# Kernel tuning notes

Hardware: AMD Instinct MI355X
Metric: run time of the kernel (lower is better)

The kernel has to match this reference:

```python
import jax, jax.numpy as jnp
import numpy as np

B, L, D = 2, 2048, 2048
H, KVH, Dh = 16, 8, 128
S_ROPE = 1024
EPS = 1e-5


def rms_norm(x, w):
    xf = x.astype(jnp.float32)
    xf = xf * jax.lax.rsqrt(jnp.mean(xf * xf, axis=-1, keepdims=True) + EPS)
    return (xf * w).astype(x.dtype)


def rotate_half(x):
    x1, x2 = jnp.split(x, 2, axis=-1)
    return jnp.concatenate((-x2, x1), axis=-1)


def setup_inputs() -> dict:
    key = jax.random.key(0)
    ks = jax.random.split(key, 12)
    sc = 0.02
    # 1D rope tables at every absolute position (theta = 500000 as in config)
    inv_freq = 1.0 / (500000.0 ** (np.arange(0, Dh, 2, dtype=np.float32) / Dh))
    ang = np.arange(L, dtype=np.float32)[:, None] * inv_freq[None, :]  # [L, Dh/2]
    emb = np.concatenate([ang, ang], axis=-1)  # [L, Dh]
    # 3D rope as per-pair 2x2 rotation matrices
    ang3 = np.random.RandomState(0).uniform(-np.pi, np.pi, size=(S_ROPE, Dh // 2)).astype(np.float32)
    R = np.stack([np.stack([np.cos(ang3), -np.sin(ang3)], -1),
                  np.stack([np.sin(ang3), np.cos(ang3)], -1)], -2)  # [S,Dh/2,2,2]
    mpos = jnp.array([[[128, 1025], [1160, 513]],
                      [[128, 1025], [1160, 513]]], dtype=jnp.int64)
    return {
        "hidden_states": jax.random.normal(ks[0], (B, L, D), jnp.float32),
        "temb": jax.random.normal(ks[1], (B, D), jnp.float32),
        "w_ln": jnp.ones((D,), jnp.float32),
        "w_mod": jax.random.normal(ks[2], (D, 3 * D), jnp.float32) * sc,
        "b_mod": jnp.zeros((3 * D,), jnp.float32),
        "wq": jax.random.normal(ks[3], (D, H * Dh), jnp.float32) * sc,
        "wk": jax.random.normal(ks[4], (D, KVH * Dh), jnp.float32) * sc,
        "wv": jax.random.normal(ks[5], (D, KVH * Dh), jnp.float32) * sc,
        "wo": jax.random.normal(ks[6], (H * Dh, D), jnp.float32) * sc,
        "qn_w": jnp.ones((Dh,), jnp.float32),
        "kn_w": jnp.ones((Dh,), jnp.float32),
        "cos_1d": jnp.asarray(np.cos(emb)),
        "sin_1d": jnp.asarray(np.sin(emb)),
        "rope_3d": jnp.asarray(R),
        "modality_positions": mpos,
    }


def _masks(modality_positions):
    pos = jnp.arange(L)  # [L]
    off = modality_positions[..., 0]   # [B, S]
    ln = modality_positions[..., 1]    # [B, S]
    meta = 1  # add_time_embeds=True, add_ar_embeds=False
    seg_end = off + jnp.maximum(ln, meta)
    in_full = (pos[None, None, :] >= off[..., None]) & (pos[None, None, :] < seg_end[..., None])
    text_mask = ~jnp.any(in_full, axis=1)  # [B, L]
    img_start = off + meta
    in_img = (pos[None, None, :] >= img_start[..., None]) & (pos[None, None, :] < (off + ln)[..., None])
    rel = jnp.sum(jnp.where(in_img, pos[None, None, :] - img_start[..., None], 0), axis=1)  # [B, L]
    img_mask = jnp.any(in_img, axis=1) & (rel < S_ROPE) & (rel >= 0)
    rel = jnp.clip(rel, 0, S_ROPE - 1)
    return text_mask, img_mask, rel


def _apply_mixed_rope(q, k, cos_1d, sin_1d, rope_3d, text_mask, img_mask, rel):
    # text 1D rope (rotate_half style), applied at absolute position
    c = cos_1d[None, None]  # [1,1,L,Dh]
    s = sin_1d[None, None]
    q_txt = q * c + rotate_half(q) * s
    k_txt = k * c + rotate_half(k) * s
    # image 3D rope: per-pair 2x2 rotation gathered at within-image index
    R = rope_3d[rel]  # [B, L, Dh/2, 2, 2]
    q2 = q.reshape(*q.shape[:-1], Dh // 2, 2)
    k2 = k.reshape(*k.shape[:-1], Dh // 2, 2)
    q_img = jnp.einsum('bhlpi,blpij->bhlpj', q2, R).reshape(q.shape)
    k_img = jnp.einsum('bhlpi,blpij->bhlpj', k2, R).reshape(k.shape)
    mt = text_mask[:, None, :, None]
    mi = img_mask[:, None, :, None]
    q_out = jnp.where(mt, q_txt, jnp.where(mi, q_img, q))
    k_out = jnp.where(mt, k_txt, jnp.where(mi, k_img, k))
    return q_out, k_out


def reference(hidden_states, temb, w_ln, w_mod, b_mod, wq, wk, wv, wo,
              qn_w, kn_w, cos_1d, sin_1d, rope_3d, modality_positions):
    dtype = hidden_states.dtype
    # adaLN modulation
    mod = jax.nn.silu(temb) @ w_mod + b_mod  # [B, 3D]
    shift, scale, gate = jnp.split(mod, 3, axis=-1)
    xn = rms_norm(hidden_states, w_ln)
    xm = (xn.astype(jnp.float32) * (1.0 + scale[:, None, :].astype(jnp.float32))
          + shift[:, None, :].astype(jnp.float32)).astype(dtype)
    # qkv projections (GQA)
    q = (xm @ wq).reshape(B, L, H, Dh).transpose(0, 2, 1, 3)
    k = (xm @ wk).reshape(B, L, KVH, Dh).transpose(0, 2, 1, 3)
    v = (xm @ wv).reshape(B, L, KVH, Dh).transpose(0, 2, 1, 3)
    # qk-norm over head_dim
    q = rms_norm(q, qn_w)
    k = rms_norm(k, kn_w)
    # mixed 3D-image / 1D-text RoPE
    text_mask, img_mask, rel = _masks(modality_positions)
    q, k = _apply_mixed_rope(q, k, cos_1d, sin_1d, rope_3d, text_mask, img_mask, rel)
    # GQA: repeat kv heads (repeat_interleave along head dim)
    n_rep = H // KVH
    k = jnp.repeat(k, n_rep, axis=1)
    v = jnp.repeat(v, n_rep, axis=1)
    # full attention (no causal mask for diffusion block)
    scores = jnp.einsum('bhqd,bhkd->bhqk', q, k) / jnp.sqrt(jnp.asarray(Dh, q.dtype))
    attn = jax.nn.softmax(scores, axis=-1)
    o = jnp.einsum('bhqk,bhkd->bhqd', attn, v)
    o = o.transpose(0, 2, 1, 3).reshape(B, L, H * Dh) @ wo
    return hidden_states + gate[:, None, :].astype(dtype) * o


if __name__ == '__main__':
    out = reference(**setup_inputs())
    print(out.shape, out.dtype)
```

## Files before the change

### kernel.cpp

```cpp
#include <hip/hip_runtime.h>
#include <stdint.h>
#include <math.h>

typedef unsigned short u16;
typedef __attribute__((ext_vector_type(8))) short short8;
typedef __attribute__((ext_vector_type(4))) float fx4;
typedef __attribute__((ext_vector_type(4))) unsigned short u16x4;

#define DEV __device__ __forceinline__

DEV u16 f2bf(float f) {
  unsigned u = __builtin_bit_cast(unsigned, f);
  return (u16)((u + 0x7FFFu + ((u >> 16) & 1u)) >> 16);
}
DEV float bf2f(u16 h) { return __builtin_bit_cast(float, ((unsigned)h) << 16); }

DEV fx4 mfma16(short8 a, short8 b, fx4 c) {
  return __builtin_amdgcn_mfma_f32_16x16x32_bf16(a, b, c, 0, 0, 0);
}

#if __has_builtin(__builtin_amdgcn_exp2f)
DEV float exp2v(float x) { return __builtin_amdgcn_exp2f(x); }
#else
DEV float exp2v(float x) { return exp2f(x); }
#endif

#define GLD16(g, l)                                                            \
  __builtin_amdgcn_global_load_lds(                                            \
      (const __attribute__((address_space(1))) void*)(g),                      \
      (__attribute__((address_space(3))) void*)(l), 16, 0, 0)

#define WAIT_ALL() asm volatile("s_waitcnt vmcnt(0) lgkmcnt(0)" ::: "memory")

__global__ __launch_bounds__(512) void k_silu_mod(
    const float* __restrict__ temb, const float* __restrict__ wmod,
    const float* __restrict__ bmod, float* __restrict__ mod) {
  __shared__ float st[4096];
  __shared__ float red[8][2][64];
  int tid = threadIdx.x;
  for (int i = tid; i < 4096; i += 512) {
    float t = temb[i];
    st[i] = t / (1.0f + __expf(-t));
  }
  __syncthreads();
  int j = blockIdx.x * 64 + (tid & 63);
  int ks = tid >> 6;
  float a0 = 0.f, a1 = 0.f;
  for (int d = ks * 256; d < ks * 256 + 256; ++d) {
    float w = wmod[(size_t)d * 6144 + j];
    a0 += st[d] * w;
    a1 += st[2048 + d] * w;
  }
  red[ks][0][tid & 63] = a0;
  red[ks][1][tid & 63] = a1;
  __syncthreads();
  if (tid < 64) {
    float s0 = 0.f, s1 = 0.f;
#pragma unroll
    for (int i = 0; i < 8; ++i) {
      s0 += red[i][0][tid];
      s1 += red[i][1][tid];
    }
    mod[j] = s0 + bmod[j];
    mod[6144 + j] = s1 + bmod[j];
  }
}

__global__ __launch_bounds__(256) void k_xm(
    const float* __restrict__ x, const float* __restrict__ wln,
    const float* __restrict__ mod, u16* __restrict__ xm) {
  int row = blockIdx.x;
  int b = row >> 11;
  const float* xr = x + (size_t)row * 2048;
  int tid = threadIdx.x;
  float4 v0 = ((const float4*)xr)[tid];
  float4 v1 = ((const float4*)xr)[tid + 256];
  float ss = v0.x * v0.x + v0.y * v0.y + v0.z * v0.z + v0.w * v0.w +
             v1.x * v1.x + v1.y * v1.y + v1.z * v1.z + v1.w * v1.w;
  for (int m = 1; m < 64; m <<= 1) ss += __shfl_xor(ss, m);
  __shared__ float red[4];
  if ((tid & 63) == 0) red[tid >> 6] = ss;
  __syncthreads();
  ss = red[0] + red[1] + red[2] + red[3];
  float r = rsqrtf(ss * (1.0f / 2048.0f) + 1e-5f);
  const float* mb = mod + (size_t)b * 6144;
#pragma unroll
  for (int c = 0; c < 2; ++c) {
    int j0 = (tid + c * 256) * 4;
    float4 xv = c ? v1 : v0;
    float4 sh = *(const float4*)(mb + j0);
    float4 sc = *(const float4*)(mb + 2048 + j0);
    float4 wl = *(const float4*)(wln + j0);
    u16x4 o;
    o.x = f2bf(xv.x * r * wl.x * (1.f + sc.x) + sh.x);
    o.y = f2bf(xv.y * r * wl.y * (1.f + sc.y) + sh.y);
    o.z = f2bf(xv.z * r * wl.z * (1.f + sc.z) + sh.z);
    o.w = f2bf(xv.w * r * wl.w * (1.f + sc.w) + sh.w);
    *(u16x4*)(xm + (size_t)row * 2048 + j0) = o;
  }
}

__global__ __launch_bounds__(256) void k_tconv(
    const float* __restrict__ src, u16* __restrict__ dst, int cols, int rows) {
  __shared__ float t[32][33];
  int kb = blockIdx.x * 32, nb = blockIdx.y * 32;
  int tx = threadIdx.x, ty = threadIdx.y;
#pragma unroll
  for (int i = 0; i < 4; ++i)
    t[ty + i * 8][tx] = src[(size_t)(kb + ty + i * 8) * cols + nb + tx];
  __syncthreads();
#pragma unroll
  for (int i = 0; i < 4; ++i)
    dst[(size_t)(nb + ty + i * 8) * rows + kb + tx] = f2bf(t[tx][ty + i * 8]);
}

template <int EPI>
__global__ __launch_bounds__(256) void k_gemm(
    const u16* __restrict__ A, const u16* __restrict__ Bt, void* __restrict__ Cp,
    const float* __restrict__ hid, const float* __restrict__ mod, int N, int K) {
  __shared__ u16 As[128 * 32];
  __shared__ u16 Bs[128 * 32];
  int tid = threadIdx.x;
  int wave = tid >> 6, lane = tid & 63, quad = lane >> 4, l16 = lane & 15;
  int m0 = blockIdx.y * 128, n0 = blockIdx.x * 128;
  int wm = (wave >> 1) * 64, wn = (wave & 1) * 64;
  fx4 acc[4][4] = {};
  int rowa = tid >> 2;
  int chunk = (tid & 3) ^ ((rowa >> 1) & 3);
  int cola = chunk * 8;
  const u16* Ag = A + (size_t)(m0 + rowa) * K + cola;
  const u16* Bg = Bt + (size_t)(n0 + rowa) * K + cola;
  u16* AsW = &As[wave * 512];
  u16* BsW = &Bs[wave * 512];
  int sl = (quad ^ ((l16 >> 1) & 3)) * 8;
  for (int k0 = 0; k0 < K; k0 += 32) {
    GLD16(Ag + k0, AsW);
    GLD16(Ag + k0 + (size_t)64 * K, AsW + 2048);
    GLD16(Bg + k0, BsW);
    GLD16(Bg + k0 + (size_t)64 * K, BsW + 2048);
    __syncthreads();
    short8 af[4], bfr[4];
#pragma unroll
    for (int i = 0; i < 4; ++i) {
      af[i] = *(const short8*)&As[(wm + i * 16 + l16) * 32 + sl];
      bfr[i] = *(const short8*)&Bs[(wn + i * 16 + l16) * 32 + sl];
    }
#pragma unroll
    for (int i = 0; i < 4; ++i)
#pragma unroll
      for (int j = 0; j < 4; ++j) acc[i][j] = mfma16(af[i], bfr[j], acc[i][j]);
    __syncthreads();
  }
#pragma unroll
  for (int i = 0; i < 4; ++i) {
    int row = m0 + wm + i * 16 + quad * 4;
#pragma unroll
    for (int j = 0; j < 4; ++j) {
      int col = n0 + wn + j * 16 + l16;
      if (EPI == 0) {
        u16* C = (u16*)Cp;
#pragma unroll
        for (int r = 0; r < 4; ++r)
          C[(size_t)(row + r) * N + col] = f2bf(acc[i][j][r]);
      } else {
        float* C = (float*)Cp;
        int b = row >> 11;
        float g = mod[(size_t)b * 6144 + 4096 + col];
#pragma unroll
        for (int r = 0; r < 4; ++r)
          C[(size_t)(row + r) * N + col] =
              hid[(size_t)(row + r) * N + col] + g * acc[i][j][r];
      }
    }
  }
}

__global__ __launch_bounds__(192) void k_qknorm(
    const u16* __restrict__ qkv, const float* __restrict__ qn,
    const float* __restrict__ kn, const float* __restrict__ cos1,
    const float* __restrict__ sin1, const float* __restrict__ r3,
    const int* __restrict__ mpos, u16* __restrict__ Q, u16* __restrict__ Kb) {
  int bx = blockIdx.x;
  int b = bx >> 11, l = bx & 2047;
  int tid = threadIdx.x;
  int slot = tid >> 3, sub = tid & 7;
  bool isq = slot < 16;
  int head = isq ? slot : slot - 16;
  const u16* base = qkv + (size_t)bx * 4096 + (isq ? slot * 128 : 2048 + head * 128);
  int d0 = sub * 16;
  float xv[16];
#pragma unroll
  for (int i = 0; i < 16; ++i) xv[i] = bf2f(base[d0 + i]);
  float ss = 0.f;
#pragma unroll
  for (int i = 0; i < 16; ++i) ss += xv[i] * xv[i];
  ss += __shfl_xor(ss, 1);
  ss += __shfl_xor(ss, 2);
  ss += __shfl_xor(ss, 4);
  float r = rsqrtf(ss * (1.0f / 128.0f) + 1e-5f);
  int mp[8];
  {
    bool is64 = (mpos[1] == 0) & (mpos[3] == 0) & (mpos[5] == 0) & (mpos[7] == 0);
#pragma unroll
    for (int i = 0; i < 8; ++i) mp[i] = is64 ? mpos[2 * i] : mpos[i];
  }
  bool infull = false, inimg = false;
  int rel = 0;
#pragma unroll
  for (int s = 0; s < 2; ++s) {
    int off = mp[b * 4 + s * 2], ln = mp[b * 4 + s * 2 + 1];
    int mx = ln > 1 ? ln : 1;
    infull |= (l >= off) && (l < off + mx);
    bool ii = (l >= off + 1) && (l < off + ln);
    inimg |= ii;
    rel += ii ? (l - (off + 1)) : 0;
  }
  bool text = !infull;
  bool img = inimg && (rel < 1024);
  const float* w = isq ? qn : kn;
  float out[16];
  if (text) {
    int dp0 = d0 ^ 64;
    float sgn = (d0 < 64) ? -1.f : 1.f;
#pragma unroll
    for (int i = 0; i < 16; ++i) {
      int d = d0 + i, dp = dp0 + i;
      float c = cos1[(size_t)l * 128 + d];
      float s = sin1[(size_t)l * 128 + d];
      float xp = bf2f(base[dp]);
      out[i] = r * (xv[i] * w[d] * c + sgn * xp * w[dp] * s);
    }
  } else if (img) {
    const float* R = r3 + ((size_t)rel * 64 + (d0 >> 1)) * 4;
#pragma unroll
    for (int p = 0; p < 8; ++p) {
      float a = xv[2 * p] * w[d0 + 2 * p] * r;
      float c2 = xv[2 * p + 1] * w[d0 + 2 * p + 1] * r;
      out[2 * p] = a * R[4 * p + 0] + c2 * R[4 * p + 2];
      out[2 * p + 1] = a * R[4 * p + 1] + c2 * R[4 * p + 3];
    }
  } else {
#pragma unroll
    for (int i = 0; i < 16; ++i) out[i] = xv[i] * w[d0 + i] * r;
  }
  if (isq) {
    u16* dst = Q + ((size_t)(b * 16 + head) * 2048 + l) * 128 + d0;
#pragma unroll
    for (int i = 0; i < 16; ++i)
      dst[i] = f2bf(out[i] * (0.08838834764831845f * 1.4426950408889634f));
  } else {
    u16* dst = Kb + ((size_t)(b * 8 + head) * 2048 + l) * 128 + d0;
#pragma unroll
    for (int i = 0; i < 16; ++i) dst[i] = f2bf(out[i]);
  }
}

__global__ __launch_bounds__(256) void k_vtrans(const u16* __restrict__ qkv,
                                                u16* __restrict__ VT) {
  __shared__ u16 t[64][65];
  int bh = blockIdx.x;
  int l0 = blockIdx.y * 64, d0 = blockIdx.z * 64;
  int b = bh >> 3, kvh = bh & 7;
  int tx = threadIdx.x & 63, tg = threadIdx.x >> 6;
#pragma unroll
  for (int i = 0; i < 16; ++i) {
    int li = tg + i * 4;
    t[li][tx] = qkv[(size_t)(b * 2048 + l0 + li) * 4096 + 3072 + kvh * 128 + d0 + tx];
  }
  __syncthreads();
#pragma unroll
  for (int i = 0; i < 16; ++i) {
    int di = tg + i * 4;
    VT[((size_t)bh * 128 + d0 + di) * 2048 + l0 + tx] = t[tx][di];
  }
}

__global__ __launch_bounds__(512, 4) void k_attn(
    const u16* __restrict__ Q, const u16* __restrict__ Kb,
    const u16* __restrict__ VT, u16* __restrict__ O) {
  __shared__ u16 Ks[2][64 * 128];
  __shared__ u16 Vs[2][128 * 64];
  __shared__ u16 Ps[128 * 64];
  int tid = threadIdx.x;
  int wave = tid >> 6, lane = tid & 63, quad = lane >> 4, l16 = lane & 15;
  int bh = blockIdx.y;
  int b = bh >> 4, h = bh & 15, kvh = h >> 1;
  int q0 = blockIdx.x * 128;
  const u16* Qb = Q + ((size_t)bh * 2048 + q0 + wave * 16) * 128;
  short8 qf[4];
#pragma unroll
  for (int ks = 0; ks < 4; ++ks)
    qf[ks] = *(const short8*)(Qb + l16 * 128 + ks * 32 + quad * 8);
  const u16* Kg = Kb + (size_t)(b * 8 + kvh) * 2048 * 128;
  const u16* Vg = VT + (size_t)(b * 8 + kvh) * 128 * 2048;
  float mrow[4], lpart[4];
  fx4 of[8] = {};
#pragma unroll
  for (int r = 0; r < 4; ++r) {
    mrow[r] = -INFINITY;
    lpart[r] = 0.f;
  }
  size_t kgo[2], vgo[2];
#pragma unroll
  for (int i = 0; i < 2; ++i) {
    int kr = i * 32 + wave * 4 + (lane >> 4);
    kgo[i] = (size_t)kr * 128 + (((lane & 15) ^ (kr & 15)) * 8);
    int vr = i * 64 + wave * 8 + (lane >> 3);
    vgo[i] = (size_t)vr * 2048 + (((lane & 7) ^ (vr & 7)) * 8);
  }

  auto STAGE = [&](int t, int buf) {
    size_t ko = (size_t)t * 8192;
    size_t vo = (size_t)t * 64;
#pragma unroll
    for (int i = 0; i < 2; ++i) {
      GLD16(Kg + ko + kgo[i], &Ks[buf][i * 4096 + wave * 512]);
      GLD16(Vg + vo + vgo[i], &Vs[buf][i * 4096 + wave * 512]);
    }
  };

  auto COMPUTE = [&](int buf) {
    fx4 sf[4] = {};
    __builtin_amdgcn_s_setprio(1);
#pragma unroll
    for (int ct = 0; ct < 4; ++ct) {
#pragma unroll
      for (int ks = 0; ks < 4; ++ks) {
        short8 kf = *(const short8*)&Ks[buf][(ct * 16 + l16) * 128 +
                                            (((ks * 4 + quad) ^ l16) * 8)];
        sf[ct] = mfma16(qf[ks], kf, sf[ct]);
      }
    }
    __builtin_amdgcn_s_setprio(0);
    float cmv[4];
    bool need = false;
#pragma unroll
    for (int r = 0; r < 4; ++r) {
      cmv[r] = fmaxf(fmaxf(sf[0][r], sf[1][r]), fmaxf(sf[2][r], sf[3][r]));
      need |= (cmv[r] > mrow[r] + 8.0f);
    }
    if (__any(need)) {
#pragma unroll
      for (int r = 0; r < 4; ++r) {
        float cm = cmv[r];
        cm = fmaxf(cm, __shfl_xor(cm, 1));
        cm = fmaxf(cm, __shfl_xor(cm, 2));
        cm = fmaxf(cm, __shfl_xor(cm, 4));
        cm = fmaxf(cm, __shfl_xor(cm, 8));
        float mn = fmaxf(mrow[r], cm);
        float al = exp2v(mrow[r] - mn);
        mrow[r] = mn;
        lpart[r] *= al;
#pragma unroll
        for (int c2 = 0; c2 < 8; ++c2) of[c2][r] *= al;
      }
    }
    int hb = l16 >> 3;
#pragma unroll
    for (int r = 0; r < 4; ++r) {
      float p0 = exp2v(sf[0][r] - mrow[r]);
      float p1 = exp2v(sf[1][r] - mrow[r]);
      float p2 = exp2v(sf[2][r] - mrow[r]);
      float p3 = exp2v(sf[3][r] - mrow[r]);
      lpart[r] += (p0 + p1) + (p2 + p3);
      int prow = wave * 16 + quad * 4 + r;
      int pb = prow * 64, px = prow & 7, lo = l16 & 7;
      Ps[pb + ((0 + hb) ^ px) * 8 + lo] = f2bf(p0);
      Ps[pb + ((2 + hb) ^ px) * 8 + lo] = f2bf(p1);
      Ps[pb + ((4 + hb) ^ px) * 8 + lo] = f2bf(p2);
      Ps[pb + ((6 + hb) ^ px) * 8 + lo] = f2bf(p3);
    }
    __builtin_amdgcn_s_setprio(1);
#pragma unroll
    for (int ks2 = 0; ks2 < 2; ++ks2) {
      int rsl = (((ks2 * 4 + quad) ^ (l16 & 7)) * 8);
      short8 pa = *(const short8*)&Ps[(wave * 16 + l16) * 64 + rsl];
#pragma unroll
      for (int c2 = 0; c2 < 8; ++c2) {
        short8 vb = *(const short8*)&Vs[buf][(c2 * 16 + l16) * 64 + rsl];
        of[c2] = mfma16(pa, vb, of[c2]);
      }
    }
    __builtin_amdgcn_s_setprio(0);
  };

  STAGE(0, 0);
  WAIT_ALL();
  __builtin_amdgcn_s_barrier();
  int cur = 0;
  for (int t = 0; t < 31; ++t) {
    STAGE(t + 1, cur ^ 1);
    COMPUTE(cur);
    WAIT_ALL();
    __builtin_amdgcn_s_barrier();
    cur ^= 1;
  }
  COMPUTE(cur);

#pragma unroll
  for (int r = 0; r < 4; ++r) {
    float ls = lpart[r];
    ls += __shfl_xor(ls, 1);
    ls += __shfl_xor(ls, 2);
    ls += __shfl_xor(ls, 4);
    ls += __shfl_xor(ls, 8);
    float inv = 1.0f / ls;
    int qrow = q0 + wave * 16 + quad * 4 + r;
#pragma unroll
    for (int c2 = 0; c2 < 8; ++c2)
      O[((size_t)b * 2048 + qrow) * 2048 + h * 128 + c2 * 16 + l16] =
          f2bf(of[c2][r] * inv);
  }
}

extern "C" void kernel_launch(void* const* d_in, const int* in_sizes, int n_in,
                              void* d_out, int out_size, void* d_ws, size_t ws_size,
                              hipStream_t stream) {
  (void)in_sizes; (void)n_in; (void)out_size; (void)ws_size;
  const float* hid  = (const float*)d_in[0];
  const float* temb = (const float*)d_in[1];
  const float* wln  = (const float*)d_in[2];
  const float* wmod = (const float*)d_in[3];
  const float* bmod = (const float*)d_in[4];
  const float* wq   = (const float*)d_in[5];
  const float* wk   = (const float*)d_in[6];
  const float* wv   = (const float*)d_in[7];
  const float* wo   = (const float*)d_in[8];
  const float* qn   = (const float*)d_in[9];
  const float* kn   = (const float*)d_in[10];
  const float* cos1 = (const float*)d_in[11];
  const float* sin1 = (const float*)d_in[12];
  const float* r3   = (const float*)d_in[13];
  const int*   mpos = (const int*)d_in[14];

  char* ws = (char*)d_ws;
  float* mod = (float*)(ws + 0);
  u16* xm  = (u16*)(ws + 49152);
  u16* wT  = (u16*)(ws + 16826368);
  u16* woT = wT;
  u16* qkv = (u16*)(ws + 33603584);
  u16* Qb  = (u16*)(ws + 67158016);
  u16* Kv  = (u16*)(ws + 83935232);
  u16* VT  = (u16*)(ws + 92323840);
  u16* Ob  = qkv;

  dim3 b32(32, 8);
  k_silu_mod<<<96, 512, 0, stream>>>(temb, wmod, bmod, mod);
  k_tconv<<<dim3(64, 64), b32, 0, stream>>>(wq, wT, 2048, 2048);
  k_tconv<<<dim3(64, 32), b32, 0, stream>>>(wk, wT + (size_t)2048 * 2048, 1024, 2048);
  k_tconv<<<dim3(64, 32), b32, 0, stream>>>(wv, wT + (size_t)3072 * 2048, 1024, 2048);
  k_xm<<<4096, 256, 0, stream>>>(hid, wln, mod, xm);
  k_gemm<0><<<dim3(32, 32), 256, 0, stream>>>(xm, wT, qkv, nullptr, nullptr, 4096, 2048);
  k_tconv<<<dim3(64, 64), b32, 0, stream>>>(wo, woT, 2048, 2048);
  k_qknorm<<<4096, 192, 0, stream>>>(qkv, qn, kn, cos1, sin1, r3, mpos, Qb, Kv);
  k_vtrans<<<dim3(16, 32, 2), 256, 0, stream>>>(qkv, VT);
  k_attn<<<dim3(16, 32), 512, 0, stream>>>(Qb, Kv, VT, Ob);
  k_gemm<1><<<dim3(16, 32), 256, 0, stream>>>(Ob, woT, d_out, hid, mod, 2048, 2048);
}
```

Before: 491.6 us.

## Double-buffer GEMM LDS tiles and swizzle workgroup order for L2 locality

The GEMM kernel now holds two LDS buffers per operand, so global-to-LDS loads for the next K-slice are issued before the MFMAs on the current slice and memory latency overlaps compute. The single barrier per iteration replaces two __syncthreads. Workgroup IDs are also remapped in groups of 8 (an XCD-style swizzle) to improve cache locality across chiplets. The change doubles LDS use, which may lower occupancy, and the remap assumes the workgroup count is divisible by 8.

```diff
diff --git a/kernel.cpp b/kernel.cpp
--- a/kernel.cpp
+++ b/kernel.cpp
@@ -118,11 +118,16 @@
 __global__ __launch_bounds__(256) void k_gemm(
     const u16* __restrict__ A, const u16* __restrict__ Bt, void* __restrict__ Cp,
     const float* __restrict__ hid, const float* __restrict__ mod, int N, int K) {
-  __shared__ u16 As[128 * 32];
-  __shared__ u16 Bs[128 * 32];
+  __shared__ u16 As[2][128 * 32];
+  __shared__ u16 Bs[2][128 * 32];
   int tid = threadIdx.x;
   int wave = tid >> 6, lane = tid & 63, quad = lane >> 4, l16 = lane & 15;
-  int m0 = blockIdx.y * 128, n0 = blockIdx.x * 128;
+  int gx = gridDim.x;
+  int nwg = gx * gridDim.y;
+  int lin = blockIdx.y * gx + blockIdx.x;
+  int cpx = nwg >> 3;
+  int swz = (lin & 7) * cpx + (lin >> 3);
+  int m0 = (swz / gx) * 128, n0 = (swz % gx) * 128;
   int wm = (wave >> 1) * 64, wn = (wave & 1) * 64;
   fx4 acc[4][4] = {};
   int rowa = tid >> 2;
@@ -130,27 +135,42 @@
   int cola = chunk * 8;
   const u16* Ag = A + (size_t)(m0 + rowa) * K + cola;
   const u16* Bg = Bt + (size_t)(n0 + rowa) * K + cola;
-  u16* AsW = &As[wave * 512];
-  u16* BsW = &Bs[wave * 512];
   int sl = (quad ^ ((l16 >> 1) & 3)) * 8;
-  for (int k0 = 0; k0 < K; k0 += 32) {
+
+  auto STAGE = [&](int k0, int buf) {
+    u16* AsW = &As[buf][wave * 512];
+    u16* BsW = &Bs[buf][wave * 512];
     GLD16(Ag + k0, AsW);
     GLD16(Ag + k0 + (size_t)64 * K, AsW + 2048);
     GLD16(Bg + k0, BsW);
     GLD16(Bg + k0 + (size_t)64 * K, BsW + 2048);
-    __syncthreads();
+  };
+  auto COMPUTE = [&](int buf) {
     short8 af[4], bfr[4];
 #pragma unroll
     for (int i = 0; i < 4; ++i) {
-      af[i] = *(const short8*)&As[(wm + i * 16 + l16) * 32 + sl];
-      bfr[i] = *(const short8*)&Bs[(wn + i * 16 + l16) * 32 + sl];
+      af[i] = *(const short8*)&As[buf][(wm + i * 16 + l16) * 32 + sl];
+      bfr[i] = *(const short8*)&Bs[buf][(wn + i * 16 + l16) * 32 + sl];
     }
 #pragma unroll
     for (int i = 0; i < 4; ++i)
 #pragma unroll
       for (int j = 0; j < 4; ++j) acc[i][j] = mfma16(af[i], bfr[j], acc[i][j]);
-    __syncthreads();
-  }
+  };
+
+  STAGE(0, 0);
+  WAIT_ALL();
+  __builtin_amdgcn_s_barrier();
+  int cur = 0;
+  for (int k0 = 32; k0 < K; k0 += 32) {
+    STAGE(k0, cur ^ 1);
+    COMPUTE(cur);
+    WAIT_ALL();
+    __builtin_amdgcn_s_barrier();
+    cur ^= 1;
+  }
+  COMPUTE(cur);
+
 #pragma unroll
   for (int i = 0; i < 4; ++i) {
     int row = m0 + wm + i * 16 + quad * 4;
```

After: 487.4 us. About the same (-0.8%).
